# Optimization experiments

Hardware: AMD Instinct MI355X
Metric: run time of the kernel (lower is better)

## Reference

```python
import jax, jax.numpy as jnp
import numpy as np

N_VARS = 1_000_000
N_CLAUSES = 4_000_000
N_EDGES = 12_000_000


def setup_inputs() -> dict:
    key = jax.random.key(0)
    k1, k2, k3 = jax.random.split(key, 3)
    preds = jax.random.uniform(k1, (N_VARS,), dtype=jnp.float32)
    lits = jax.random.randint(k2, (N_EDGES,), 0, 2 * N_VARS, dtype=jnp.int32)
    clauses = jax.random.randint(k3, (N_EDGES,), 0, N_CLAUSES, dtype=jnp.int32)
    return {
        "preds": preds,
        "lits": lits,
        "clauses": clauses,
        "n_vars": N_VARS,
        "n_clauses": N_CLAUSES,
    }


def reference(preds, lits, clauses, n_vars, n_clauses):
    # Map literal index to variable index: lits < n_vars -> positive literal,
    # lits >= n_vars -> negated literal of variable (lits - n_vars).
    is_pos = lits < n_vars
    var_idx = jnp.where(is_pos, lits, lits - n_vars)
    pval = preds[var_idx]                                   # gather [n_edges]
    # positive literal satisfied if pred >= 0.5, negated if pred < 0.5
    satisfied = jnp.where(is_pos, pval >= 0.5, pval < 0.5).astype(jnp.float32)
    # scatter-add satisfaction flags into per-clause bins, then threshold to bool
    clause_hits = jax.ops.segment_sum(satisfied, clauses, num_segments=n_clauses)
    clause_sat = clause_hits > 0                            # [n_clauses] bool
    n_sat = clause_sat.sum().astype(jnp.float32)
    loss = (jnp.float32(n_clauses) - n_sat) / jnp.float32(n_vars)
    return loss
```

## Files before the change

### kernel.cpp

```cpp
#include <hip/hip_runtime.h>

#define BLOCK 256


__global__ void zero_ws(uint4* __restrict__ ws, const int* __restrict__ n_clauses_p) {
    const int nc = *n_clauses_p;
    const int total16 = (64 + ((nc + 15) & ~15)) >> 4;
    const uint4 z = {0u, 0u, 0u, 0u};
    int i = blockIdx.x * blockDim.x + threadIdx.x;
    const int stride = gridDim.x * blockDim.x;
    for (; i < total16; i += stride) ws[i] = z;
}

__device__ __forceinline__ void edge_one(int lit, int cls, int nv,
                                         const float* __restrict__ preds,
                                         unsigned char* __restrict__ sat) {
    const bool pos = lit < nv;
    const int v = pos ? lit : lit - nv;
    const float p = preds[v];
    if (pos == (p >= 0.5f)) sat[cls] = (unsigned char)1;
}

__global__ void scatter_sat(const int* __restrict__ lits,
                            const int* __restrict__ clauses,
                            const float* __restrict__ preds,
                            unsigned char* __restrict__ sat,
                            int n_edges,
                            const int* __restrict__ n_vars_p) {
    const int nv = *n_vars_p;
    const int tid = blockIdx.x * blockDim.x + threadIdx.x;
    const int stride = gridDim.x * blockDim.x;
    const int n4 = n_edges >> 2;

    const int4* __restrict__ l4 = reinterpret_cast<const int4*>(lits);
    const int4* __restrict__ c4 = reinterpret_cast<const int4*>(clauses);

    for (int i = tid; i < n4; i += stride) {
        const int4 l = l4[i];
        const int4 c = c4[i];
        edge_one(l.x, c.x, nv, preds, sat);
        edge_one(l.y, c.y, nv, preds, sat);
        edge_one(l.z, c.z, nv, preds, sat);
        edge_one(l.w, c.w, nv, preds, sat);
    }
    for (int i = (n4 << 2) + tid; i < n_edges; i += stride) {
        edge_one(lits[i], clauses[i], nv, preds, sat);
    }
}

__global__ void reduce_finalize(const uint4* __restrict__ sat16,
                                unsigned* __restrict__ nsat,
                                unsigned* __restrict__ done,
                                float* __restrict__ out,
                                const int* __restrict__ n_clauses_p,
                                const int* __restrict__ n_vars_p) {
    const int nc = *n_clauses_p;
    const int n16 = (nc + 15) >> 4;
    const int tid = blockIdx.x * blockDim.x + threadIdx.x;
    const int stride = gridDim.x * blockDim.x;

    unsigned acc = 0;
    for (int i = tid; i < n16; i += stride) {
        const uint4 v = sat16[i];
        acc += __popc(v.x & 0x01010101u) + __popc(v.y & 0x01010101u) +
               __popc(v.z & 0x01010101u) + __popc(v.w & 0x01010101u);
    }

    #pragma unroll
    for (int off = 32; off > 0; off >>= 1) acc += __shfl_down(acc, off);

    __shared__ unsigned smem[BLOCK / 64];
    const int lane = threadIdx.x & 63;
    const int wid  = threadIdx.x >> 6;
    if (lane == 0) smem[wid] = acc;
    __syncthreads();

    if (threadIdx.x == 0) {
        unsigned bsum = 0;
        #pragma unroll
        for (int w = 0; w < BLOCK / 64; ++w) bsum += smem[w];
        atomicAdd(nsat, bsum);
        __threadfence();
        const unsigned ticket = atomicAdd(done, 1u);
        if (ticket == (unsigned)(gridDim.x - 1)) {
            const unsigned total = atomicAdd(nsat, 0u);
            const float nv = (float)(*n_vars_p);
            *out = ((float)nc - (float)total) / nv;
        }
    }
}

extern "C" void kernel_launch(void* const* d_in, const int* in_sizes, int n_in,
                              void* d_out, int out_size, void* d_ws, size_t ws_size,
                              hipStream_t stream) {
    const float* preds   = (const float*)d_in[0];
    const int*   lits    = (const int*)d_in[1];
    const int*   clauses = (const int*)d_in[2];
    const int*   nv_p    = (const int*)d_in[3];
    const int*   nc_p    = (const int*)d_in[4];
    const int    n_edges = in_sizes[1];

    float* out = (float*)d_out;
    unsigned char* ws = (unsigned char*)d_ws;
    unsigned* nsat = (unsigned*)ws;
    unsigned* done = (unsigned*)(ws + 4);
    unsigned char* sat = ws + 64;

    zero_ws<<<1024, BLOCK, 0, stream>>>((uint4*)ws, nc_p);
    scatter_sat<<<2048, BLOCK, 0, stream>>>(lits, clauses, preds, sat, n_edges, nv_p);
    reduce_finalize<<<512, BLOCK, 0, stream>>>((const uint4*)sat, nsat, done, out,
                                               nc_p, nv_p);
}
```

Baseline: 303.0 us.

## Bit-pack predictions and clause-satisfied flags to shrink gather/scatter footprint

Adds a prep pass that ballots preds>=0.5 into a 1M-bit table (125KB) so the per-edge gather hits a tiny, cache-resident array instead of the 4MB float array. The per-clause satisfied flags become a 4M-bit bitmap written with a test-then-atomicOr, replacing the byte stores, and the final reduction popcounts whole words. Costs are an extra pass over preds and atomic contention on shared bitmap words, in exchange for much smaller random-access working sets. n_vars now comes from the input array size rather than the device scalar.

Result: slower. 608.6 us (+100.9%).

```diff
diff --git a/kernel.cpp b/kernel.cpp
--- a/kernel.cpp
+++ b/kernel.cpp
@@ -1,33 +1,53 @@
 #include <hip/hip_runtime.h>
+#include <stdint.h>
 
 #define BLOCK 256
 
 
-__global__ void zero_ws(uint4* __restrict__ ws, const int* __restrict__ n_clauses_p) {
-    const int nc = *n_clauses_p;
-    const int total16 = (64 + ((nc + 15) & ~15)) >> 4;
+__global__ void prep(const float* __restrict__ preds,
+                     unsigned long long* __restrict__ predbits,
+                     uint4* __restrict__ satz,
+                     unsigned* __restrict__ hdr,
+                     int n_vars,
+                     const int* __restrict__ nc_p) {
+    const int gid = blockIdx.x * blockDim.x + threadIdx.x;
+    const int stride = gridDim.x * blockDim.x;
+
+    const int nv64 = (n_vars + 63) & ~63;
+    for (int i = gid; i < nv64; i += stride) {
+        const bool b = (i < n_vars) && (preds[i] >= 0.5f);
+        const unsigned long long m = __ballot(b);
+        if ((threadIdx.x & 63) == 0) predbits[i >> 6] = m;
+    }
+
+    const int nc = *nc_p;
+    const int satw16 = (((nc + 31) >> 5) + 3) >> 2;
     const uint4 z = {0u, 0u, 0u, 0u};
-    int i = blockIdx.x * blockDim.x + threadIdx.x;
-    const int stride = gridDim.x * blockDim.x;
-    for (; i < total16; i += stride) ws[i] = z;
+    for (int i = gid; i < satw16; i += stride) satz[i] = z;
+
+    if (gid == 0) { hdr[0] = 0u; hdr[1] = 0u; }
 }
 
 __device__ __forceinline__ void edge_one(int lit, int cls, int nv,
-                                         const float* __restrict__ preds,
-                                         unsigned char* __restrict__ sat) {
+                                         const unsigned* __restrict__ predbits,
+                                         unsigned* __restrict__ sat) {
     const bool pos = lit < nv;
     const int v = pos ? lit : lit - nv;
-    const float p = preds[v];
-    if (pos == (p >= 0.5f)) sat[cls] = (unsigned char)1;
+    const unsigned pb = predbits[v >> 5];
+    const bool pbit = ((pb >> (v & 31)) & 1u) != 0u;
+    if (pbit == pos) {
+        const unsigned w = ((unsigned)cls) >> 5;
+        const unsigned m = 1u << (cls & 31);
+        if ((sat[w] & m) == 0u)
+            atomicOr(&sat[w], m);
+    }
 }
 
 __global__ void scatter_sat(const int* __restrict__ lits,
                             const int* __restrict__ clauses,
-                            const float* __restrict__ preds,
-                            unsigned char* __restrict__ sat,
-                            int n_edges,
-                            const int* __restrict__ n_vars_p) {
-    const int nv = *n_vars_p;
+                            const unsigned* __restrict__ predbits,
+                            unsigned* __restrict__ sat,
+                            int n_edges, int n_vars) {
     const int tid = blockIdx.x * blockDim.x + threadIdx.x;
     const int stride = gridDim.x * blockDim.x;
     const int n4 = n_edges >> 2;
@@ -38,13 +58,13 @@
     for (int i = tid; i < n4; i += stride) {
         const int4 l = l4[i];
         const int4 c = c4[i];
-        edge_one(l.x, c.x, nv, preds, sat);
-        edge_one(l.y, c.y, nv, preds, sat);
-        edge_one(l.z, c.z, nv, preds, sat);
-        edge_one(l.w, c.w, nv, preds, sat);
+        edge_one(l.x, c.x, n_vars, predbits, sat);
+        edge_one(l.y, c.y, n_vars, predbits, sat);
+        edge_one(l.z, c.z, n_vars, predbits, sat);
+        edge_one(l.w, c.w, n_vars, predbits, sat);
     }
     for (int i = (n4 << 2) + tid; i < n_edges; i += stride) {
-        edge_one(lits[i], clauses[i], nv, preds, sat);
+        edge_one(lits[i], clauses[i], n_vars, predbits, sat);
     }
 }
 
@@ -52,18 +72,17 @@
                                 unsigned* __restrict__ nsat,
                                 unsigned* __restrict__ done,
                                 float* __restrict__ out,
-                                const int* __restrict__ n_clauses_p,
-                                const int* __restrict__ n_vars_p) {
-    const int nc = *n_clauses_p;
-    const int n16 = (nc + 15) >> 4;
+                                const int* __restrict__ nc_p,
+                                int n_vars) {
+    const int nc = *nc_p;
+    const int n16 = (((nc + 31) >> 5) + 3) >> 2;
     const int tid = blockIdx.x * blockDim.x + threadIdx.x;
     const int stride = gridDim.x * blockDim.x;
 
     unsigned acc = 0;
     for (int i = tid; i < n16; i += stride) {
         const uint4 v = sat16[i];
-        acc += __popc(v.x & 0x01010101u) + __popc(v.y & 0x01010101u) +
-               __popc(v.z & 0x01010101u) + __popc(v.w & 0x01010101u);
+        acc += __popc(v.x) + __popc(v.y) + __popc(v.z) + __popc(v.w);
     }
 
     #pragma unroll
@@ -84,8 +103,7 @@
         const unsigned ticket = atomicAdd(done, 1u);
         if (ticket == (unsigned)(gridDim.x - 1)) {
             const unsigned total = atomicAdd(nsat, 0u);
-            const float nv = (float)(*n_vars_p);
-            *out = ((float)nc - (float)total) / nv;
+            *out = ((float)nc - (float)total) / (float)n_vars;
         }
     }
 }
@@ -96,18 +114,24 @@
     const float* preds   = (const float*)d_in[0];
     const int*   lits    = (const int*)d_in[1];
     const int*   clauses = (const int*)d_in[2];
-    const int*   nv_p    = (const int*)d_in[3];
     const int*   nc_p    = (const int*)d_in[4];
+    const int    n_vars  = in_sizes[0];
     const int    n_edges = in_sizes[1];
 
     float* out = (float*)d_out;
     unsigned char* ws = (unsigned char*)d_ws;
-    unsigned* nsat = (unsigned*)ws;
-    unsigned* done = (unsigned*)(ws + 4);
-    unsigned char* sat = ws + 64;
+    unsigned* hdr = (unsigned*)ws;
+    unsigned long long* predbits = (unsigned long long*)(ws + 64);
+    const size_t predbits_bytes = ((size_t)((n_vars + 63) / 64)) * 8;
+    size_t satoff = 64 + predbits_bytes;
+    satoff = (satoff + 15) & ~(size_t)15;
+    unsigned* satmap = (unsigned*)(ws + satoff);
 
-    zero_ws<<<1024, BLOCK, 0, stream>>>((uint4*)ws, nc_p);
-    scatter_sat<<<2048, BLOCK, 0, stream>>>(lits, clauses, preds, sat, n_edges, nv_p);
-    reduce_finalize<<<512, BLOCK, 0, stream>>>((const uint4*)sat, nsat, done, out,
-                                               nc_p, nv_p);
+    prep<<<2048, BLOCK, 0, stream>>>(preds, predbits, (uint4*)satmap, hdr,
+                                     n_vars, nc_p);
+    scatter_sat<<<2048, BLOCK, 0, stream>>>(lits, clauses,
+                                            (const unsigned*)predbits, satmap,
+                                            n_edges, n_vars);
+    reduce_finalize<<<128, BLOCK, 0, stream>>>((const uint4*)satmap,
+                                               hdr, hdr + 1, out, nc_p, n_vars);
 }
```
